# Optimization experiments

Hardware: AMD Instinct MI355X
Metric: run time of the kernel (lower is better)

## Reference

```python
import jax, jax.numpy as jnp
import numpy as np


def setup_inputs() -> dict:
    key = jax.random.key(0)
    ks = jax.random.split(key, 18)
    V, E, H, T = 32000, 512, 1024, 256
    s_e = 1.0 / np.sqrt(E)
    s_h = 1.0 / np.sqrt(H)
    inp = {
        "encoding": jax.random.normal(ks[0], (1, H), jnp.float32),
        "tokens": jax.random.randint(ks[1], (T,), 0, V),
        "embedding": jax.random.normal(ks[2], (V, E), jnp.float32),
        "wzx_w": jax.random.normal(ks[3], (H, E), jnp.float32) * s_e,
        "wzx_b": jax.random.normal(ks[4], (H,), jnp.float32) * s_e,
        "wrx_w": jax.random.normal(ks[5], (H, E), jnp.float32) * s_e,
        "wrx_b": jax.random.normal(ks[6], (H,), jnp.float32) * s_e,
        "whx_w": jax.random.normal(ks[7], (H, E), jnp.float32) * s_e,
        "whx_b": jax.random.normal(ks[8], (H,), jnp.float32) * s_e,
        "wzh_w": jax.random.normal(ks[9], (H, H), jnp.float32) * s_h,
        "wzh_b": jax.random.normal(ks[10], (H,), jnp.float32) * s_h,
        "wrh_w": jax.random.normal(ks[11], (H, H), jnp.float32) * s_h,
        "wrh_b": jax.random.normal(ks[12], (H,), jnp.float32) * s_h,
        "whh_w": jax.random.normal(ks[13], (H, H), jnp.float32) * s_h,
        "whh_b": jax.random.normal(ks[14], (H,), jnp.float32) * s_h,
        "out_w": jax.random.normal(ks[15], (V, H), jnp.float32) * s_h,
        "out_b": jax.random.normal(ks[16], (V,), jnp.float32) * s_h,
    }
    return inp


def reference(encoding, tokens, embedding,
              wzx_w, wzx_b, wrx_w, wrx_b, whx_w, whx_b,
              wzh_w, wzh_b, wrh_w, wrh_b, whh_w, whh_b,
              out_w, out_b):
    # Teacher-forced GRU decode: tokens[t] is the 'previous word' fed at step t.
    def step(h, tok):
        e = embedding[tok][None, :]                                   # [1, E]
        z = jax.nn.sigmoid(e @ wzx_w.T + wzx_b + h @ wzh_w.T + wzh_b)  # [1, H]
        r = jax.nn.sigmoid(e @ wrx_w.T + wrx_b + h @ wrh_w.T + wrh_b)
        h_prime = jnp.tanh(e @ whx_w.T + whx_b + (r * h) @ whh_w.T + whh_b)
        h_new = (1.0 - z) * h + z * h_prime
        logits = h_new @ out_w.T + out_b                               # [1, V]
        return h_new, logits

    _, output_vectors = jax.lax.scan(step, encoding, tokens)          # [T, 1, V]
    pred_ids = jnp.argmax(output_vectors, axis=-1)                    # [T, 1]
    return output_vectors, pred_ids
```

## Files before the change

### kernel.cpp

```cpp
#include <hip/hip_runtime.h>
#include <hip/hip_bf16.h>
#include <math.h>

constexpr int T_STEPS = 256;
constexpr int HDIM    = 1024;
constexpr int EDIM    = 512;
constexpr int VDIM    = 32000;

#define RG     128
#define RROWS  8

constexpr size_t WS_BZ     = 0;
constexpr size_t WS_BR     = WS_BZ + (size_t)T_STEPS * HDIM;
constexpr size_t WS_A      = WS_BR + (size_t)T_STEPS * HDIM;
constexpr size_t WS_HPACK  = WS_A  + (size_t)T_STEPS * HDIM;
constexpr size_t WS_RHPACK = WS_HPACK + (size_t)2 * (T_STEPS + 1) * HDIM;
constexpr size_t WS_HSEQ   = WS_BZ;
constexpr size_t WS_HSEQB  = WS_BR;

typedef __attribute__((ext_vector_type(8))) short short8;
typedef __attribute__((ext_vector_type(4))) float f32x4;

__device__ __forceinline__ float sigmoidf_(float x) { return 1.0f / (1.0f + __expf(-x)); }

__device__ __forceinline__ unsigned long long pack_tv(int tag, float v) {
  return ((unsigned long long)(unsigned)tag << 32) | (unsigned long long)__float_as_uint(v);
}

__device__ __forceinline__ unsigned short f2bf(float f) {
  unsigned u = __float_as_uint(f);
  return (unsigned short)((u + 0x7FFFu + ((u >> 16) & 1u)) >> 16);
}

__device__ __forceinline__ unsigned short f2bf_fast(float f) {
  __hip_bfloat16 b = __float2bfloat16(f);
  return *reinterpret_cast<unsigned short*>(&b);
}

__device__ __forceinline__ void publish(unsigned long long* p, unsigned long long v) {
  (void)__hip_atomic_exchange(p, v, __ATOMIC_RELAXED, __HIP_MEMORY_SCOPE_AGENT);
}

__global__ __launch_bounds__(256) void k_init(const float* __restrict__ enc, float* __restrict__ ws) {
  unsigned long long* hpack  = (unsigned long long*)(ws + WS_HPACK);
  unsigned long long* rhpack = (unsigned long long*)(ws + WS_RHPACK);
  const int b = blockIdx.x, tid = threadIdx.x;
  if (b == 0) {
    for (int i = tid; i < HDIM; i += 256) hpack[i] = pack_tv(1, enc[i]);
  } else if (b <= T_STEPS) {
    unsigned long long* row = hpack + (size_t)b * HDIM;
    for (int i = tid; i < HDIM; i += 256) row[i] = 0ULL;
  } else {
    for (int i = tid; i < HDIM; i += 256) rhpack[i] = 0ULL;
  }
}

__global__ __launch_bounds__(256) void k_xproj(
    const int* __restrict__ tokens, const float* __restrict__ emb,
    const float* __restrict__ wzx, const float* __restrict__ wrx, const float* __restrict__ whx,
    const float* __restrict__ bzx, const float* __restrict__ bzh,
    const float* __restrict__ brx, const float* __restrict__ brh,
    const float* __restrict__ bhx, const float* __restrict__ bhh,
    float* __restrict__ ws) {
  __shared__ __align__(16) float es[16][EDIM];
  const int b   = blockIdx.x;
  const int t0  = (b & 15) * 16;
  const int c   = b >> 4;
  const int tid = threadIdx.x;

  {
    int row = tid >> 4;
    int kc  = (tid & 15) * 32;
    int tok = tokens[t0 + row];
    const float4* ep = (const float4*)(emb + (size_t)tok * EDIM + kc);
    float4* dst = (float4*)&es[row][kc];
    #pragma unroll
    for (int q = 0; q < 8; q++) dst[q] = ep[q];
  }
  __syncthreads();

  const int mat = c >> 2;
  const int j   = (c & 3) * 256 + tid;
  const float* W; const float* b1; const float* b2; float* Xout;
  if (mat == 0)      { W = wzx; b1 = bzx; b2 = bzh; Xout = ws + WS_BZ; }
  else if (mat == 1) { W = wrx; b1 = brx; b2 = brh; Xout = ws + WS_BR; }
  else               { W = whx; b1 = bhx; b2 = bhh; Xout = ws + WS_A;  }

  const float4* wp = (const float4*)(W + (size_t)j * EDIM);
  const float bias = b1[j] + b2[j];
  float acc[16];
  #pragma unroll
  for (int tt = 0; tt < 16; tt++) acc[tt] = 0.0f;

  for (int k4 = 0; k4 < EDIM / 4; k4++) {
    float4 w = wp[k4];
    #pragma unroll
    for (int tt = 0; tt < 16; tt++) {
      float4 e4 = *(const float4*)&es[tt][k4 * 4];
      acc[tt] += w.x * e4.x + w.y * e4.y + w.z * e4.z + w.w * e4.w;
    }
  }
  #pragma unroll
  for (int tt = 0; tt < 16; tt++)
    Xout[(size_t)(t0 + tt) * HDIM + j] = acc[tt] + bias;
}

__global__ __launch_bounds__(256) void k_recur(
    const float* __restrict__ wzh, const float* __restrict__ wrh, const float* __restrict__ whh,
    float* __restrict__ ws) {
  const int g    = blockIdx.x;
  const int tid  = threadIdx.x;
  const int lane = tid & 63;
  const int wv   = tid >> 6;
  const float* Bz = ws + WS_BZ;
  const float* Br = ws + WS_BR;
  const float* Aa = ws + WS_A;
  float* hseq = ws + WS_HSEQ;
  unsigned short* hseqb = (unsigned short*)(ws + WS_HSEQB);
  unsigned long long* hpack  = (unsigned long long*)(ws + WS_HPACK);
  unsigned long long* rhpack = (unsigned long long*)(ws + WS_RHPACK);

  const int j0 = 4 * tid;
  const int r0 = g * RROWS;

  float4 wz[RROWS], wr[RROWS], wh[RROWS];
  #pragma unroll
  for (int k = 0; k < RROWS; k++) {
    wz[k] = *(const float4*)(wzh + (size_t)(r0 + k) * HDIM + j0);
    wr[k] = *(const float4*)(wrh + (size_t)(r0 + k) * HDIM + j0);
    wh[k] = *(const float4*)(whh + (size_t)(r0 + k) * HDIM + j0);
  }

  __shared__ float redA[4][2 * RROWS];
  __shared__ float redB[4][RROWS];
  __shared__ float zs[RROWS];
  __shared__ float hloc[RROWS];
  if (tid < RROWS)
    hloc[tid] = __uint_as_float((unsigned)hpack[r0 + tid]);
  __syncthreads();

  for (int t = 0; t < T_STEPS; t++) {
    float bz_pre = 0.0f, br_pre = 0.0f, a_pre = 0.0f;
    if (tid < RROWS) {
      bz_pre = Bz[(size_t)t * HDIM + r0 + tid];
      a_pre  = Aa[(size_t)t * HDIM + r0 + tid];
    } else if (tid < 2 * RROWS) {
      br_pre = Br[(size_t)t * HDIM + r0 + (tid - RROWS)];
    }
    const unsigned long long ex = (unsigned long long)(unsigned)(t + 1);

    float hv0, hv1, hv2, hv3;
    {
      const unsigned long long* hp = hpack + (size_t)t * HDIM + j0;
      unsigned long long w0, w1, w2, w3;
      int it = 0;
      for (;;) {
        w0 = __hip_atomic_load(hp + 0, __ATOMIC_RELAXED, __HIP_MEMORY_SCOPE_AGENT);
        if ((w0 >> 32) == ex) break;
        if (++it > (1 << 20)) break;
        __builtin_amdgcn_s_sleep(2);
      }
      for (;;) {
        w1 = __hip_atomic_load(hp + 1, __ATOMIC_RELAXED, __HIP_MEMORY_SCOPE_AGENT);
        w2 = __hip_atomic_load(hp + 2, __ATOMIC_RELAXED, __HIP_MEMORY_SCOPE_AGENT);
        w3 = __hip_atomic_load(hp + 3, __ATOMIC_RELAXED, __HIP_MEMORY_SCOPE_AGENT);
        if (((w1 >> 32) == ex) & ((w2 >> 32) == ex) & ((w3 >> 32) == ex)) break;
        if (++it > (1 << 20)) break;
        __builtin_amdgcn_s_sleep(1);
      }
      hv0 = __uint_as_float((unsigned)w0);
      hv1 = __uint_as_float((unsigned)w1);
      hv2 = __uint_as_float((unsigned)w2);
      hv3 = __uint_as_float((unsigned)w3);
    }

    float pz[RROWS], pr[RROWS];
    #pragma unroll
    for (int k = 0; k < RROWS; k++) {
      pz[k] = wz[k].x * hv0 + wz[k].y * hv1 + wz[k].z * hv2 + wz[k].w * hv3;
      pr[k] = wr[k].x * hv0 + wr[k].y * hv1 + wr[k].z * hv2 + wr[k].w * hv3;
    }
    #pragma unroll
    for (int m = 32; m >= 1; m >>= 1) {
      #pragma unroll
      for (int k = 0; k < RROWS; k++) {
        pz[k] += __shfl_xor(pz[k], m);
        pr[k] += __shfl_xor(pr[k], m);
      }
    }
    if (lane == 0) {
      #pragma unroll
      for (int k = 0; k < RROWS; k++) { redA[wv][k] = pz[k]; redA[wv][RROWS + k] = pr[k]; }
    }
    __syncthreads();
    if (tid < RROWS) {
      float u = redA[0][tid] + redA[1][tid] + redA[2][tid] + redA[3][tid];
      zs[tid] = sigmoidf_(bz_pre + u);
    } else if (tid < 2 * RROWS) {
      int k = tid - RROWS;
      float u = redA[0][tid] + redA[1][tid] + redA[2][tid] + redA[3][tid];
      float r = sigmoidf_(br_pre + u);
      float rh = r * hloc[k];
      publish(&rhpack[r0 + k], pack_tv(t + 1, rh));
    }

    float rv0, rv1, rv2, rv3;
    {
      const unsigned long long* rp = rhpack + j0;
      unsigned long long w0, w1, w2, w3;
      int it = 0;
      for (;;) {
        w0 = __hip_atomic_load(rp + 0, __ATOMIC_RELAXED, __HIP_MEMORY_SCOPE_AGENT);
        if ((w0 >> 32) == ex) break;
        if (++it > (1 << 20)) break;
        __builtin_amdgcn_s_sleep(2);
      }
      for (;;) {
        w1 = __hip_atomic_load(rp + 1, __ATOMIC_RELAXED, __HIP_MEMORY_SCOPE_AGENT);
        w2 = __hip_atomic_load(rp + 2, __ATOMIC_RELAXED, __HIP_MEMORY_SCOPE_AGENT);
        w3 = __hip_atomic_load(rp + 3, __ATOMIC_RELAXED, __HIP_MEMORY_SCOPE_AGENT);
        if (((w1 >> 32) == ex) & ((w2 >> 32) == ex) & ((w3 >> 32) == ex)) break;
        if (++it > (1 << 20)) break;
        __builtin_amdgcn_s_sleep(1);
      }
      rv0 = __uint_as_float((unsigned)w0);
      rv1 = __uint_as_float((unsigned)w1);
      rv2 = __uint_as_float((unsigned)w2);
      rv3 = __uint_as_float((unsigned)w3);
    }

    float ph[RROWS];
    #pragma unroll
    for (int k = 0; k < RROWS; k++)
      ph[k] = wh[k].x * rv0 + wh[k].y * rv1 + wh[k].z * rv2 + wh[k].w * rv3;
    #pragma unroll
    for (int m = 32; m >= 1; m >>= 1) {
      #pragma unroll
      for (int k = 0; k < RROWS; k++) ph[k] += __shfl_xor(ph[k], m);
    }
    if (lane == 0) {
      #pragma unroll
      for (int k = 0; k < RROWS; k++) redB[wv][k] = ph[k];
    }
    __syncthreads();
    if (tid < RROWS) {
      float v  = redB[0][tid] + redB[1][tid] + redB[2][tid] + redB[3][tid];
      float z  = zs[tid];
      float hk = hloc[tid];
      float hp_ = tanhf(a_pre + v);
      float hn = (1.0f - z) * hk + z * hp_;
      hloc[tid] = hn;
      publish(&hpack[(size_t)(t + 1) * HDIM + r0 + tid], pack_tv(t + 2, hn));
      hseq[(size_t)t * HDIM + r0 + tid] = hn;
      hseqb[(size_t)t * HDIM + r0 + tid] = f2bf(hn);
    }
  }
}

__global__ __launch_bounds__(256) void k_gemm(
    const unsigned short* __restrict__ Abf, const float* __restrict__ outw,
    const float* __restrict__ outb, float* __restrict__ out) {
  const int tid  = threadIdx.x;
  const int lane = tid & 63;
  const int wv   = tid >> 6;
  const int n0   = blockIdx.x * 128;
  const int rA   = lane & 15;
  const int kg   = lane >> 4;

  f32x4 acc[4][8];
  #pragma unroll
  for (int i = 0; i < 4; i++)
    #pragma unroll
    for (int j = 0; j < 8; j++) acc[i][j] = (f32x4){0.f, 0.f, 0.f, 0.f};

  const int mbase = wv * 64 + rA;

  for (int k0 = 0; k0 < HDIM; k0 += 32) {
    const int ks = k0 + kg * 8;
    short8 afr[4];
    #pragma unroll
    for (int i = 0; i < 4; i++)
      afr[i] = *(const short8*)(Abf + (size_t)(mbase + i * 16) * HDIM + ks);

    short8 bfr[8];
    #pragma unroll
    for (int j = 0; j < 8; j++) {
      const float* bp = outw + (size_t)(n0 + j * 16 + rA) * HDIM + ks;
      float4 b0 = *(const float4*)(bp);
      float4 b1 = *(const float4*)(bp + 4);
      short8 s;
      s[0] = (short)f2bf_fast(b0.x); s[1] = (short)f2bf_fast(b0.y);
      s[2] = (short)f2bf_fast(b0.z); s[3] = (short)f2bf_fast(b0.w);
      s[4] = (short)f2bf_fast(b1.x); s[5] = (short)f2bf_fast(b1.y);
      s[6] = (short)f2bf_fast(b1.z); s[7] = (short)f2bf_fast(b1.w);
      bfr[j] = s;
    }

    #pragma unroll
    for (int i = 0; i < 4; i++)
      #pragma unroll
      for (int j = 0; j < 8; j++)
        acc[i][j] = __builtin_amdgcn_mfma_f32_16x16x32_bf16(afr[i], bfr[j], acc[i][j], 0, 0, 0);
  }

  float bias[8];
  #pragma unroll
  for (int j = 0; j < 8; j++) bias[j] = outb[n0 + j * 16 + rA];
  #pragma unroll
  for (int i = 0; i < 4; i++) {
    #pragma unroll
    for (int j = 0; j < 8; j++) {
      #pragma unroll
      for (int r = 0; r < 4; r++) {
        int m = wv * 64 + i * 16 + kg * 4 + r;
        out[(size_t)m * VDIM + n0 + j * 16 + rA] = acc[i][j][r] + bias[j];
      }
    }
  }
}

__global__ __launch_bounds__(256) void k_argmax(const float* __restrict__ logits,
                                                const float* __restrict__ hseqf,
                                                const float* __restrict__ outw,
                                                const float* __restrict__ outb,
                                                float* __restrict__ outids) {
  const int t = blockIdx.x;
  const int tid = threadIdx.x;
  const float* row = logits + (size_t)t * VDIM;

  float mx = -3.4e38f;
  for (int v = tid; v < VDIM; v += 256) mx = fmaxf(mx, row[v]);
  __shared__ float sm[256];
  sm[tid] = mx;
  __syncthreads();
  for (int s = 128; s > 0; s >>= 1) {
    if (tid < s) sm[tid] = fmaxf(sm[tid], sm[tid + s]);
    __syncthreads();
  }
  const float bmax = sm[0];
  __syncthreads();

  __shared__ int cand[64];
  __shared__ int cnt;
  if (tid == 0) cnt = 0;
  __syncthreads();
  const float cut = bmax - 0.25f;
  for (int v = tid; v < VDIM; v += 256) {
    if (row[v] >= cut) {
      int p = atomicAdd(&cnt, 1);
      if (p < 64) cand[p] = v;
    }
  }
  __syncthreads();
  int n = cnt < 64 ? cnt : 64;

  __shared__ float cval[64];
  if (tid < n) {
    int v = cand[tid];
    const float* w = outw + (size_t)v * HDIM;
    const float* h = hseqf + (size_t)t * HDIM;
    float s0 = 0.f, s1 = 0.f, s2 = 0.f, s3 = 0.f;
    for (int k = 0; k < HDIM; k += 4) {
      float4 wf = *(const float4*)(w + k);
      float4 hf = *(const float4*)(h + k);
      s0 += wf.x * hf.x; s1 += wf.y * hf.y; s2 += wf.z * hf.z; s3 += wf.w * hf.w;
    }
    cval[tid] = (s0 + s1) + (s2 + s3) + outb[v];
  }
  __syncthreads();
  if (tid == 0) {
    float best = -3.4e38f; int bi = 0x7FFFFFFF;
    for (int i = 0; i < n; i++) {
      float v = cval[i]; int id = cand[i];
      if (v > best || (v == best && id < bi)) { best = v; bi = id; }
    }
    outids[t] = (float)bi;
  }
}

extern "C" void kernel_launch(void* const* d_in, const int* in_sizes, int n_in,
                              void* d_out, int out_size, void* d_ws, size_t ws_size,
                              hipStream_t stream) {
  (void)in_sizes; (void)n_in; (void)out_size; (void)ws_size;
  const float* enc    = (const float*)d_in[0];
  const int*   tokens = (const int*)d_in[1];
  const float* emb    = (const float*)d_in[2];
  const float* wzx_w  = (const float*)d_in[3];
  const float* wzx_b  = (const float*)d_in[4];
  const float* wrx_w  = (const float*)d_in[5];
  const float* wrx_b  = (const float*)d_in[6];
  const float* whx_w  = (const float*)d_in[7];
  const float* whx_b  = (const float*)d_in[8];
  const float* wzh_w  = (const float*)d_in[9];
  const float* wzh_b  = (const float*)d_in[10];
  const float* wrh_w  = (const float*)d_in[11];
  const float* wrh_b  = (const float*)d_in[12];
  const float* whh_w  = (const float*)d_in[13];
  const float* whh_b  = (const float*)d_in[14];
  const float* out_w  = (const float*)d_in[15];
  const float* out_b  = (const float*)d_in[16];
  float* ws  = (float*)d_ws;
  float* out = (float*)d_out;

  k_init<<<dim3(T_STEPS + 2), dim3(256), 0, stream>>>(enc, ws);
  k_xproj<<<dim3(192), dim3(256), 0, stream>>>(tokens, emb, wzx_w, wrx_w, whx_w,
                                               wzx_b, wzh_b, wrx_b, wrh_b, whx_b, whh_b, ws);
  k_recur<<<dim3(RG), dim3(256), 0, stream>>>(wzh_w, wrh_w, whh_w, ws);
  k_gemm<<<dim3(VDIM / 128), dim3(256), 0, stream>>>((const unsigned short*)(ws + WS_HSEQB),
                                                     out_w, out_b, out);
  k_argmax<<<dim3(T_STEPS), dim3(256), 0, stream>>>(out, ws + WS_HSEQ, out_w, out_b,
                                                    out + (size_t)T_STEPS * VDIM);
}
```

Baseline: 1.452 ms.

## Overlap output GEMM with GRU recurrence via chunked flag-waiting GEMM blocks in one kernel

Merges the recurrence and the vocab-projection GEMM into one persistent launch. The first 128 blocks run the recurrence at raised priority, and extra GEMM blocks each wait for a 64-step chunk of hidden states before computing their logits tile. GEMM blocks read h directly from the tagged hpack buffer and convert it to bf16, so the separate bf16 hidden-state copy is dropped. Init and input-projection kernels are also fused into one launch. This hides GEMM time behind the serial recurrence, but spinning GEMM blocks may occupy CUs and slow the recurrence; correctness relies on recurrence blocks being resident.

Result: slower. 2.353 ms (+62.0%).

```diff
diff --git a/kernel.cpp b/kernel.cpp
--- a/kernel.cpp
+++ b/kernel.cpp
@@ -9,6 +9,9 @@
 
 #define RG     128
 #define RROWS  8
+#define NBN    125
+#define NCH    4
+#define GEMMB  (NBN * NCH)
 
 constexpr size_t WS_BZ     = 0;
 constexpr size_t WS_BR     = WS_BZ + (size_t)T_STEPS * HDIM;
@@ -16,7 +19,6 @@
 constexpr size_t WS_HPACK  = WS_A  + (size_t)T_STEPS * HDIM;
 constexpr size_t WS_RHPACK = WS_HPACK + (size_t)2 * (T_STEPS + 1) * HDIM;
 constexpr size_t WS_HSEQ   = WS_BZ;
-constexpr size_t WS_HSEQB  = WS_BR;
 
 typedef __attribute__((ext_vector_type(8))) short short8;
 typedef __attribute__((ext_vector_type(4))) float f32x4;
@@ -25,11 +27,6 @@
 
 __device__ __forceinline__ unsigned long long pack_tv(int tag, float v) {
   return ((unsigned long long)(unsigned)tag << 32) | (unsigned long long)__float_as_uint(v);
-}
-
-__device__ __forceinline__ unsigned short f2bf(float f) {
-  unsigned u = __float_as_uint(f);
-  return (unsigned short)((u + 0x7FFFu + ((u >> 16) & 1u)) >> 16);
 }
 
 __device__ __forceinline__ unsigned short f2bf_fast(float f) {
@@ -37,37 +34,33 @@
   return *reinterpret_cast<unsigned short*>(&b);
 }
 
-__device__ __forceinline__ void publish(unsigned long long* p, unsigned long long v) {
-  (void)__hip_atomic_exchange(p, v, __ATOMIC_RELAXED, __HIP_MEMORY_SCOPE_AGENT);
-}
-
-__global__ __launch_bounds__(256) void k_init(const float* __restrict__ enc, float* __restrict__ ws) {
-  unsigned long long* hpack  = (unsigned long long*)(ws + WS_HPACK);
-  unsigned long long* rhpack = (unsigned long long*)(ws + WS_RHPACK);
-  const int b = blockIdx.x, tid = threadIdx.x;
-  if (b == 0) {
-    for (int i = tid; i < HDIM; i += 256) hpack[i] = pack_tv(1, enc[i]);
-  } else if (b <= T_STEPS) {
-    unsigned long long* row = hpack + (size_t)b * HDIM;
-    for (int i = tid; i < HDIM; i += 256) row[i] = 0ULL;
-  } else {
-    for (int i = tid; i < HDIM; i += 256) rhpack[i] = 0ULL;
-  }
-}
-
-__global__ __launch_bounds__(256) void k_xproj(
+__global__ __launch_bounds__(256) void k_pre(
+    const float* __restrict__ enc,
     const int* __restrict__ tokens, const float* __restrict__ emb,
     const float* __restrict__ wzx, const float* __restrict__ wrx, const float* __restrict__ whx,
     const float* __restrict__ bzx, const float* __restrict__ bzh,
     const float* __restrict__ brx, const float* __restrict__ brh,
     const float* __restrict__ bhx, const float* __restrict__ bhh,
     float* __restrict__ ws) {
+  const int tid = threadIdx.x;
+  if (blockIdx.x >= 192) {
+    unsigned long long* hpack  = (unsigned long long*)(ws + WS_HPACK);
+    unsigned long long* rhpack = (unsigned long long*)(ws + WS_RHPACK);
+    const int b2 = blockIdx.x - 192;
+    if (b2 == 0) {
+      for (int i = tid; i < HDIM; i += 256) hpack[i] = pack_tv(1, enc[i]);
+    } else if (b2 <= T_STEPS) {
+      unsigned long long* row = hpack + (size_t)b2 * HDIM;
+      for (int i = tid; i < HDIM; i += 256) row[i] = 0ULL;
+    } else {
+      for (int i = tid; i < HDIM; i += 256) rhpack[i] = 0ULL;
+    }
+    return;
+  }
   __shared__ __align__(16) float es[16][EDIM];
   const int b   = blockIdx.x;
   const int t0  = (b & 15) * 16;
   const int c   = b >> 4;
-  const int tid = threadIdx.x;
-
   {
     int row = tid >> 4;
     int kc  = (tid & 15) * 32;
@@ -81,13 +74,13 @@
 
   const int mat = c >> 2;
   const int j   = (c & 3) * 256 + tid;
-  const float* W; const float* b1; const float* b2; float* Xout;
-  if (mat == 0)      { W = wzx; b1 = bzx; b2 = bzh; Xout = ws + WS_BZ; }
-  else if (mat == 1) { W = wrx; b1 = brx; b2 = brh; Xout = ws + WS_BR; }
-  else               { W = whx; b1 = bhx; b2 = bhh; Xout = ws + WS_A;  }
+  const float* W; const float* b1; const float* b2p; float* Xout;
+  if (mat == 0)      { W = wzx; b1 = bzx; b2p = bzh; Xout = ws + WS_BZ; }
+  else if (mat == 1) { W = wrx; b1 = brx; b2p = brh; Xout = ws + WS_BR; }
+  else               { W = whx; b1 = bhx; b2p = bhh; Xout = ws + WS_A;  }
 
   const float4* wp = (const float4*)(W + (size_t)j * EDIM);
-  const float bias = b1[j] + b2[j];
+  const float bias = b1[j] + b2p[j];
   float acc[16];
   #pragma unroll
   for (int tt = 0; tt < 16; tt++) acc[tt] = 0.0f;
@@ -105,187 +98,212 @@
     Xout[(size_t)(t0 + tt) * HDIM + j] = acc[tt] + bias;
 }
 
-__global__ __launch_bounds__(256) void k_recur(
+__global__ __launch_bounds__(256, 4) void k_main(
     const float* __restrict__ wzh, const float* __restrict__ wrh, const float* __restrict__ whh,
-    float* __restrict__ ws) {
-  const int g    = blockIdx.x;
+    const float* __restrict__ outw, const float* __restrict__ outb,
+    float* __restrict__ ws, float* __restrict__ out) {
   const int tid  = threadIdx.x;
   const int lane = tid & 63;
   const int wv   = tid >> 6;
-  const float* Bz = ws + WS_BZ;
-  const float* Br = ws + WS_BR;
-  const float* Aa = ws + WS_A;
-  float* hseq = ws + WS_HSEQ;
-  unsigned short* hseqb = (unsigned short*)(ws + WS_HSEQB);
   unsigned long long* hpack  = (unsigned long long*)(ws + WS_HPACK);
   unsigned long long* rhpack = (unsigned long long*)(ws + WS_RHPACK);
 
-  const int j0 = 4 * tid;
-  const int r0 = g * RROWS;
-
-  float4 wz[RROWS], wr[RROWS], wh[RROWS];
-  #pragma unroll
-  for (int k = 0; k < RROWS; k++) {
-    wz[k] = *(const float4*)(wzh + (size_t)(r0 + k) * HDIM + j0);
-    wr[k] = *(const float4*)(wrh + (size_t)(r0 + k) * HDIM + j0);
-    wh[k] = *(const float4*)(whh + (size_t)(r0 + k) * HDIM + j0);
-  }
-
-  __shared__ float redA[4][2 * RROWS];
-  __shared__ float redB[4][RROWS];
-  __shared__ float zs[RROWS];
-  __shared__ float hloc[RROWS];
-  if (tid < RROWS)
-    hloc[tid] = __uint_as_float((unsigned)hpack[r0 + tid]);
-  __syncthreads();
-
-  for (int t = 0; t < T_STEPS; t++) {
-    float bz_pre = 0.0f, br_pre = 0.0f, a_pre = 0.0f;
-    if (tid < RROWS) {
-      bz_pre = Bz[(size_t)t * HDIM + r0 + tid];
-      a_pre  = Aa[(size_t)t * HDIM + r0 + tid];
-    } else if (tid < 2 * RROWS) {
-      br_pre = Br[(size_t)t * HDIM + r0 + (tid - RROWS)];
-    }
-    const unsigned long long ex = (unsigned long long)(unsigned)(t + 1);
-
-    float hv0, hv1, hv2, hv3;
-    {
-      const unsigned long long* hp = hpack + (size_t)t * HDIM + j0;
-      unsigned long long w0, w1, w2, w3;
-      int it = 0;
-      for (;;) {
-        w0 = __hip_atomic_load(hp + 0, __ATOMIC_RELAXED, __HIP_MEMORY_SCOPE_AGENT);
-        if ((w0 >> 32) == ex) break;
-        if (++it > (1 << 20)) break;
-        __builtin_amdgcn_s_sleep(2);
-      }
-      for (;;) {
-        w1 = __hip_atomic_load(hp + 1, __ATOMIC_RELAXED, __HIP_MEMORY_SCOPE_AGENT);
-        w2 = __hip_atomic_load(hp + 2, __ATOMIC_RELAXED, __HIP_MEMORY_SCOPE_AGENT);
-        w3 = __hip_atomic_load(hp + 3, __ATOMIC_RELAXED, __HIP_MEMORY_SCOPE_AGENT);
-        if (((w1 >> 32) == ex) & ((w2 >> 32) == ex) & ((w3 >> 32) == ex)) break;
-        if (++it > (1 << 20)) break;
-        __builtin_amdgcn_s_sleep(1);
-      }
-      hv0 = __uint_as_float((unsigned)w0);
-      hv1 = __uint_as_float((unsigned)w1);
-      hv2 = __uint_as_float((unsigned)w2);
-      hv3 = __uint_as_float((unsigned)w3);
-    }
-
-    float pz[RROWS], pr[RROWS];
+  if (blockIdx.x < RG) {
+    __builtin_amdgcn_s_setprio(1);
+    const int g  = blockIdx.x;
+    const float* Bz = ws + WS_BZ;
+    const float* Br = ws + WS_BR;
+    const float* Aa = ws + WS_A;
+    float* hseq = ws + WS_HSEQ;
+
+    const int j0 = 4 * tid;
+    const int r0 = g * RROWS;
+
+    float4 wz[RROWS], wr[RROWS], wh[RROWS];
     #pragma unroll
     for (int k = 0; k < RROWS; k++) {
-      pz[k] = wz[k].x * hv0 + wz[k].y * hv1 + wz[k].z * hv2 + wz[k].w * hv3;
-      pr[k] = wr[k].x * hv0 + wr[k].y * hv1 + wr[k].z * hv2 + wr[k].w * hv3;
-    }
-    #pragma unroll
-    for (int m = 32; m >= 1; m >>= 1) {
+      wz[k] = *(const float4*)(wzh + (size_t)(r0 + k) * HDIM + j0);
+      wr[k] = *(const float4*)(wrh + (size_t)(r0 + k) * HDIM + j0);
+      wh[k] = *(const float4*)(whh + (size_t)(r0 + k) * HDIM + j0);
+    }
+
+    __shared__ float redA[4][2 * RROWS];
+    __shared__ float redB[4][RROWS];
+    __shared__ float zs[RROWS];
+    __shared__ float hloc[RROWS];
+    if (tid < RROWS)
+      hloc[tid] = __uint_as_float((unsigned)hpack[r0 + tid]);
+    __syncthreads();
+
+    for (int t = 0; t < T_STEPS; t++) {
+      float bz_pre = 0.0f, br_pre = 0.0f, a_pre = 0.0f;
+      if (tid < RROWS) {
+        bz_pre = Bz[(size_t)t * HDIM + r0 + tid];
+        a_pre  = Aa[(size_t)t * HDIM + r0 + tid];
+      } else if (tid < 2 * RROWS) {
+        br_pre = Br[(size_t)t * HDIM + r0 + (tid - RROWS)];
+      }
+      const unsigned long long ex = (unsigned long long)(unsigned)(t + 1);
+
+      float hv0, hv1, hv2, hv3;
+      {
+        const unsigned long long* hp = hpack + (size_t)t * HDIM + j0;
+        unsigned long long w0, w1, w2, w3;
+        int it = 0;
+        for (;;) {
+          w0 = __hip_atomic_load(hp + 0, __ATOMIC_RELAXED, __HIP_MEMORY_SCOPE_AGENT);
+          if ((w0 >> 32) == ex) break;
+          if (++it > (1 << 20)) break;
+          __builtin_amdgcn_s_sleep(2);
+        }
+        for (;;) {
+          w1 = __hip_atomic_load(hp + 1, __ATOMIC_RELAXED, __HIP_MEMORY_SCOPE_AGENT);
+          w2 = __hip_atomic_load(hp + 2, __ATOMIC_RELAXED, __HIP_MEMORY_SCOPE_AGENT);
+          w3 = __hip_atomic_load(hp + 3, __ATOMIC_RELAXED, __HIP_MEMORY_SCOPE_AGENT);
+          if (((w1 >> 32) == ex) & ((w2 >> 32) == ex) & ((w3 >> 32) == ex)) break;
+          if (++it > (1 << 20)) break;
+          __builtin_amdgcn_s_sleep(1);
+        }
+        hv0 = __uint_as_float((unsigned)w0);
+        hv1 = __uint_as_float((unsigned)w1);
+        hv2 = __uint_as_float((unsigned)w2);
+        hv3 = __uint_as_float((unsigned)w3);
+      }
+
+      float pz[RROWS], pr[RROWS];
       #pragma unroll
       for (int k = 0; k < RROWS; k++) {
-        pz[k] += __shfl_xor(pz[k], m);
-        pr[k] += __shfl_xor(pr[k], m);
-      }
-    }
-    if (lane == 0) {
-      #pragma unroll
-      for (int k = 0; k < RROWS; k++) { redA[wv][k] = pz[k]; redA[wv][RROWS + k] = pr[k]; }
-    }
-    __syncthreads();
-    if (tid < RROWS) {
-      float u = redA[0][tid] + redA[1][tid] + redA[2][tid] + redA[3][tid];
-      zs[tid] = sigmoidf_(bz_pre + u);
-    } else if (tid < 2 * RROWS) {
-      int k = tid - RROWS;
-      float u = redA[0][tid] + redA[1][tid] + redA[2][tid] + redA[3][tid];
-      float r = sigmoidf_(br_pre + u);
-      float rh = r * hloc[k];
-      publish(&rhpack[r0 + k], pack_tv(t + 1, rh));
-    }
-
-    float rv0, rv1, rv2, rv3;
-    {
-      const unsigned long long* rp = rhpack + j0;
-      unsigned long long w0, w1, w2, w3;
-      int it = 0;
-      for (;;) {
-        w0 = __hip_atomic_load(rp + 0, __ATOMIC_RELAXED, __HIP_MEMORY_SCOPE_AGENT);
-        if ((w0 >> 32) == ex) break;
-        if (++it > (1 << 20)) break;
-        __builtin_amdgcn_s_sleep(2);
-      }
-      for (;;) {
-        w1 = __hip_atomic_load(rp + 1, __ATOMIC_RELAXED, __HIP_MEMORY_SCOPE_AGENT);
-        w2 = __hip_atomic_load(rp + 2, __ATOMIC_RELAXED, __HIP_MEMORY_SCOPE_AGENT);
-        w3 = __hip_atomic_load(rp + 3, __ATOMIC_RELAXED, __HIP_MEMORY_SCOPE_AGENT);
-        if (((w1 >> 32) == ex) & ((w2 >> 32) == ex) & ((w3 >> 32) == ex)) break;
-        if (++it > (1 << 20)) break;
-        __builtin_amdgcn_s_sleep(1);
-      }
-      rv0 = __uint_as_float((unsigned)w0);
-      rv1 = __uint_as_float((unsigned)w1);
-      rv2 = __uint_as_float((unsigned)w2);
-      rv3 = __uint_as_float((unsigned)w3);
-    }
-
-    float ph[RROWS];
-    #pragma unroll
-    for (int k = 0; k < RROWS; k++)
-      ph[k] = wh[k].x * rv0 + wh[k].y * rv1 + wh[k].z * rv2 + wh[k].w * rv3;
-    #pragma unroll
-    for (int m = 32; m >= 1; m >>= 1) {
-      #pragma unroll
-      for (int k = 0; k < RROWS; k++) ph[k] += __shfl_xor(ph[k], m);
-    }
-    if (lane == 0) {
-      #pragma unroll
-      for (int k = 0; k < RROWS; k++) redB[wv][k] = ph[k];
-    }
-    __syncthreads();
-    if (tid < RROWS) {
-      float v  = redB[0][tid] + redB[1][tid] + redB[2][tid] + redB[3][tid];
-      float z  = zs[tid];
-      float hk = hloc[tid];
-      float hp_ = tanhf(a_pre + v);
-      float hn = (1.0f - z) * hk + z * hp_;
-      hloc[tid] = hn;
-      publish(&hpack[(size_t)(t + 1) * HDIM + r0 + tid], pack_tv(t + 2, hn));
-      hseq[(size_t)t * HDIM + r0 + tid] = hn;
-      hseqb[(size_t)t * HDIM + r0 + tid] = f2bf(hn);
-    }
-  }
-}
-
-__global__ __launch_bounds__(256) void k_gemm(
-    const unsigned short* __restrict__ Abf, const float* __restrict__ outw,
-    const float* __restrict__ outb, float* __restrict__ out) {
-  const int tid  = threadIdx.x;
-  const int lane = tid & 63;
-  const int wv   = tid >> 6;
-  const int n0   = blockIdx.x * 128;
-  const int rA   = lane & 15;
-  const int kg   = lane >> 4;
-
-  f32x4 acc[4][8];
+        pz[k] = wz[k].x * hv0 + wz[k].y * hv1 + wz[k].z * hv2 + wz[k].w * hv3;
+        pr[k] = wr[k].x * hv0 + wr[k].y * hv1 + wr[k].z * hv2 + wr[k].w * hv3;
+      }
+      #pragma unroll
+      for (int m = 32; m >= 1; m >>= 1) {
+        #pragma unroll
+        for (int k = 0; k < RROWS; k++) {
+          pz[k] += __shfl_xor(pz[k], m);
+          pr[k] += __shfl_xor(pr[k], m);
+        }
+      }
+      if (lane == 0) {
+        #pragma unroll
+        for (int k = 0; k < RROWS; k++) { redA[wv][k] = pz[k]; redA[wv][RROWS + k] = pr[k]; }
+      }
+      __syncthreads();
+      if (tid < RROWS) {
+        float u = redA[0][tid] + redA[1][tid] + redA[2][tid] + redA[3][tid];
+        zs[tid] = sigmoidf_(bz_pre + u);
+      } else if (tid < 2 * RROWS) {
+        int k = tid - RROWS;
+        float u = redA[0][tid] + redA[1][tid] + redA[2][tid] + redA[3][tid];
+        float r = sigmoidf_(br_pre + u);
+        float rh = r * hloc[k];
+        __hip_atomic_store(&rhpack[r0 + k], pack_tv(t + 1, rh),
+                           __ATOMIC_RELAXED, __HIP_MEMORY_SCOPE_AGENT);
+      }
+
+      float rv0, rv1, rv2, rv3;
+      {
+        const unsigned long long* rp = rhpack + j0;
+        unsigned long long w0, w1, w2, w3;
+        int it = 0;
+        for (;;) {
+          w0 = __hip_atomic_load(rp + 0, __ATOMIC_RELAXED, __HIP_MEMORY_SCOPE_AGENT);
+          if ((w0 >> 32) == ex) break;
+          if (++it > (1 << 20)) break;
+          __builtin_amdgcn_s_sleep(2);
+        }
+        for (;;) {
+          w1 = __hip_atomic_load(rp + 1, __ATOMIC_RELAXED, __HIP_MEMORY_SCOPE_AGENT);
+          w2 = __hip_atomic_load(rp + 2, __ATOMIC_RELAXED, __HIP_MEMORY_SCOPE_AGENT);
+          w3 = __hip_atomic_load(rp + 3, __ATOMIC_RELAXED, __HIP_MEMORY_SCOPE_AGENT);
+          if (((w1 >> 32) == ex) & ((w2 >> 32) == ex) & ((w3 >> 32) == ex)) break;
+          if (++it > (1 << 20)) break;
+          __builtin_amdgcn_s_sleep(1);
+        }
+        rv0 = __uint_as_float((unsigned)w0);
+        rv1 = __uint_as_float((unsigned)w1);
+        rv2 = __uint_as_float((unsigned)w2);
+        rv3 = __uint_as_float((unsigned)w3);
+      }
+
+      float ph[RROWS];
+      #pragma unroll
+      for (int k = 0; k < RROWS; k++)
+        ph[k] = wh[k].x * rv0 + wh[k].y * rv1 + wh[k].z * rv2 + wh[k].w * rv3;
+      #pragma unroll
+      for (int m = 32; m >= 1; m >>= 1) {
+        #pragma unroll
+        for (int k = 0; k < RROWS; k++) ph[k] += __shfl_xor(ph[k], m);
+      }
+      if (lane == 0) {
+        #pragma unroll
+        for (int k = 0; k < RROWS; k++) redB[wv][k] = ph[k];
+      }
+      __syncthreads();
+      if (tid < RROWS) {
+        float v  = redB[0][tid] + redB[1][tid] + redB[2][tid] + redB[3][tid];
+        float z  = zs[tid];
+        float hk = hloc[tid];
+        float hp_ = tanhf(a_pre + v);
+        float hn = (1.0f - z) * hk + z * hp_;
+        hloc[tid] = hn;
+        __hip_atomic_store(&hpack[(size_t)(t + 1) * HDIM + r0 + tid], pack_tv(t + 2, hn),
+                           __ATOMIC_RELAXED, __HIP_MEMORY_SCOPE_AGENT);
+        hseq[(size_t)t * HDIM + r0 + tid] = hn;
+      }
+    }
+    return;
+  }
+
+  const int b  = blockIdx.x - RG;
+  const int c  = b / NBN;
+  const int nb = b - c * NBN;
+  const int n0 = nb * 256;
+  const int m0 = c * 64;
+
+  {
+    const unsigned long long thr = ((unsigned long long)(unsigned)(64 * (c + 1) + 1)) << 32;
+    const unsigned long long* prow = hpack + (size_t)(64 * (c + 1)) * HDIM;
+    const int g = tid & 127;
+    int it = 0;
+    for (;;) {
+      unsigned long long w = __hip_atomic_load(prow + (size_t)g * RROWS,
+                                               __ATOMIC_RELAXED, __HIP_MEMORY_SCOPE_AGENT);
+      int ok = (w >= thr) | (it > (1 << 17));
+      if (__syncthreads_and(ok)) break;
+      ++it;
+      __builtin_amdgcn_s_sleep(32);
+    }
+  }
+
+  const int rA  = lane & 15;
+  const int kg  = lane >> 4;
+  const int nw0 = n0 + wv * 64;
+
+  f32x4 acc[4][4];
   #pragma unroll
   for (int i = 0; i < 4; i++)
     #pragma unroll
-    for (int j = 0; j < 8; j++) acc[i][j] = (f32x4){0.f, 0.f, 0.f, 0.f};
-
-  const int mbase = wv * 64 + rA;
+    for (int j = 0; j < 4; j++) acc[i][j] = (f32x4){0.f, 0.f, 0.f, 0.f};
 
   for (int k0 = 0; k0 < HDIM; k0 += 32) {
     const int ks = k0 + kg * 8;
     short8 afr[4];
     #pragma unroll
-    for (int i = 0; i < 4; i++)
-      afr[i] = *(const short8*)(Abf + (size_t)(mbase + i * 16) * HDIM + ks);
-
-    short8 bfr[8];
-    #pragma unroll
-    for (int j = 0; j < 8; j++) {
-      const float* bp = outw + (size_t)(n0 + j * 16 + rA) * HDIM + ks;
+    for (int mi = 0; mi < 4; mi++) {
+      const unsigned long long* ap = hpack + (size_t)(m0 + mi * 16 + rA + 1) * HDIM + ks;
+      short8 s;
+      #pragma unroll
+      for (int e = 0; e < 8; e++) {
+        unsigned long long w = __hip_atomic_load(ap + e, __ATOMIC_RELAXED, __HIP_MEMORY_SCOPE_AGENT);
+        s[e] = (short)f2bf_fast(__uint_as_float((unsigned)w));
+      }
+      afr[mi] = s;
+    }
+    short8 bfr[4];
+    #pragma unroll
+    for (int nj = 0; nj < 4; nj++) {
+      const float* bp = outw + (size_t)(nw0 + nj * 16 + rA) * HDIM + ks;
       float4 b0 = *(const float4*)(bp);
       float4 b1 = *(const float4*)(bp + 4);
       short8 s;
@@ -293,27 +311,26 @@
       s[2] = (short)f2bf_fast(b0.z); s[3] = (short)f2bf_fast(b0.w);
       s[4] = (short)f2bf_fast(b1.x); s[5] = (short)f2bf_fast(b1.y);
       s[6] = (short)f2bf_fast(b1.z); s[7] = (short)f2bf_fast(b1.w);
-      bfr[j] = s;
-    }
-
-    #pragma unroll
-    for (int i = 0; i < 4; i++)
-      #pragma unroll
-      for (int j = 0; j < 8; j++)
-        acc[i][j] = __builtin_amdgcn_mfma_f32_16x16x32_bf16(afr[i], bfr[j], acc[i][j], 0, 0, 0);
-  }
-
-  float bias[8];
+      bfr[nj] = s;
+    }
+    #pragma unroll
+    for (int mi = 0; mi < 4; mi++)
+      #pragma unroll
+      for (int nj = 0; nj < 4; nj++)
+        acc[mi][nj] = __builtin_amdgcn_mfma_f32_16x16x32_bf16(afr[mi], bfr[nj], acc[mi][nj], 0, 0, 0);
+  }
+
+  float bias[4];
   #pragma unroll
-  for (int j = 0; j < 8; j++) bias[j] = outb[n0 + j * 16 + rA];
+  for (int nj = 0; nj < 4; nj++) bias[nj] = outb[nw0 + nj * 16 + rA];
   #pragma unroll
-  for (int i = 0; i < 4; i++) {
-    #pragma unroll
-    for (int j = 0; j < 8; j++) {
+  for (int mi = 0; mi < 4; mi++) {
+    #pragma unroll
+    for (int nj = 0; nj < 4; nj++) {
       #pragma unroll
       for (int r = 0; r < 4; r++) {
-        int m = wv * 64 + i * 16 + kg * 4 + r;
-        out[(size_t)m * VDIM + n0 + j * 16 + rA] = acc[i][j][r] + bias[j];
+        int m = m0 + mi * 16 + kg * 4 + r;
+        out[(size_t)m * VDIM + nw0 + nj * 16 + rA] = acc[mi][nj][r] + bias[nj];
       }
     }
   }
@@ -402,12 +419,11 @@
   float* ws  = (float*)d_ws;
   float* out = (float*)d_out;
 
-  k_init<<<dim3(T_STEPS + 2), dim3(256), 0, stream>>>(enc, ws);
-  k_xproj<<<dim3(192), dim3(256), 0, stream>>>(tokens, emb, wzx_w, wrx_w, whx_w,
-                                               wzx_b, wzh_b, wrx_b, wrh_b, whx_b, whh_b, ws);
-  k_recur<<<dim3(RG), dim3(256), 0, stream>>>(wzh_w, wrh_w, whh_w, ws);
-  k_gemm<<<dim3(VDIM / 128), dim3(256), 0, stream>>>((const unsigned short*)(ws + WS_HSEQB),
-                                                     out_w, out_b, out);
+  k_pre<<<dim3(192 + T_STEPS + 2), dim3(256), 0, stream>>>(
+      enc, tokens, emb, wzx_w, wrx_w, whx_w,
+      wzx_b, wzh_b, wrx_b, wrh_b, whx_b, whh_b, ws);
+  k_main<<<dim3(RG + GEMMB), dim3(256), 0, stream>>>(wzh_w, wrh_w, whh_w,
+                                                     out_w, out_b, ws, out);
   k_argmax<<<dim3(T_STEPS), dim3(256), 0, stream>>>(out, ws + WS_HSEQ, out_w, out_b,
                                                     out + (size_t)T_STEPS * VDIM);
 }
```
